# Kernel optimization log

Hardware: AMD Instinct MI355X
Metric: run time of the kernel (lower is better)

## Reference

```python
import jax, jax.numpy as jnp
import numpy as np


def setup_inputs() -> dict:
    key = jax.random.key(0)
    ks = jax.random.split(key, 7)
    E = 768; CH = 3; PS = 16; B = 128; P = 196
    return {
        "x": jax.random.normal(ks[0], (B, P, E), dtype=jnp.float32),
        "We": jax.random.normal(ks[1], (CH * PS * PS, E), dtype=jnp.float32) * (1.0 / np.sqrt(E)),
        "be": jax.random.normal(ks[2], (CH * PS * PS,), dtype=jnp.float32) * 0.01,
        "filter_re": jax.random.normal(ks[3], (1, 1, 1, PS, PS), dtype=jnp.float32),
        "filter_im": jax.random.normal(ks[4], (1, 1, 1, PS, PS), dtype=jnp.float32),
        "Wd": jax.random.normal(ks[5], (E, CH * PS * PS), dtype=jnp.float32) * (1.0 / np.sqrt(CH * PS * PS)),
        "bd": jax.random.normal(ks[6], (E,), dtype=jnp.float32) * 0.01,
        "ch": 3,
        "patch_size": 16,
    }


def reference(x, We, be, filter_re, filter_im, Wd, bd, ch, patch_size):
    # encode: [b,p,E] -> [b,p,ch*ps*ps]
    h = jnp.einsum('bpe,ce->bpc', x, We) + be
    b, p, _ = h.shape
    h = h.reshape(b, p, ch, patch_size, patch_size)
    # batched 2D FFT over the two trailing patch dims
    hf = jnp.fft.fft2(h, axes=(-2, -1))
    filt = (filter_re + 1j * filter_im).astype(hf.dtype)  # [1,1,1,ps,ps]
    r = jnp.fft.ifft2(hf * filt, axes=(-2, -1))
    a = jnp.abs(r).reshape(b, p, ch * patch_size * patch_size)
    # decode: [b,p,ch*ps*ps] -> [b,p,E]
    return jnp.einsum('bpc,ec->bpe', a, Wd) + bd
```

## Files before the change

kernel.cpp:

```cpp
#include <hip/hip_runtime.h>

typedef short short8 __attribute__((ext_vector_type(8)));
typedef unsigned short ushort8 __attribute__((ext_vector_type(8)));
typedef float f32x4 __attribute__((ext_vector_type(4)));

__device__ __forceinline__ unsigned short f32_to_bf16(float f) {
  unsigned u = __float_as_uint(f);
  unsigned r = 0x7fffu + ((u >> 16) & 1u);
  return (unsigned short)((u + r) >> 16);
}
__device__ __forceinline__ float bf16_to_f32(unsigned short h) {
  return __uint_as_float(((unsigned)h) << 16);
}

__global__ void cvt_f32_bf16(const float* __restrict__ s,
                             unsigned short* __restrict__ d, int n8) {
  int i = blockIdx.x * blockDim.x + threadIdx.x;
  if (i >= n8) return;
  const float4* sp = (const float4*)s;
  float4 a = sp[2 * i], b = sp[2 * i + 1];
  ushort8 o;
  o[0] = f32_to_bf16(a.x); o[1] = f32_to_bf16(a.y);
  o[2] = f32_to_bf16(a.z); o[3] = f32_to_bf16(a.w);
  o[4] = f32_to_bf16(b.x); o[5] = f32_to_bf16(b.y);
  o[6] = f32_to_bf16(b.z); o[7] = f32_to_bf16(b.w);
  ((ushort8*)d)[i] = o;
}

__device__ __forceinline__ void gload_lds16(const void* g, void* l) {
  auto* gp = (const __attribute__((address_space(1))) uint32_t*)((uintptr_t)g);
  auto* lp = (__attribute__((address_space(3))) uint32_t*)(uint32_t)(uintptr_t)l;
  __builtin_amdgcn_global_load_lds(gp, lp, 16, 0, 0);
}

template <int OUT_BF16>
__global__ __launch_bounds__(256) void gemm_bt(
    const unsigned short* __restrict__ A, const unsigned short* __restrict__ B,
    const float* __restrict__ bias, void* __restrict__ out,
    int M, int N, int K, int nbx) {
  __shared__ __align__(16) unsigned short As[2][128 * 64];
  __shared__ __align__(16) unsigned short Bs[2][128 * 64];

  const int tid = threadIdx.x;
  const int lane = tid & 63;
  const int wid = tid >> 6;
  const int wr = wid >> 1, wc = wid & 1;

  const int nwg = gridDim.x;
  const int cpx = nwg >> 3;
  const int bid = blockIdx.x;
  const int lid = (bid & 7) * cpx + (bid >> 3);
  const int m0 = (lid / nbx) * 128, n0 = (lid % nbx) * 128;

  const int lr8 = lane >> 3;
  const int swk = ((lane & 7) ^ lr8) * 8;

  f32x4 acc[4][4] = {};

  auto STAGE = [&](int buf, int k0) {
#pragma unroll
    for (int c = 0; c < 4; ++c) {
      const int rowc = wid * 32 + c * 8;
      gload_lds16(A + (size_t)(m0 + rowc + lr8) * K + (k0 + swk),
                  &As[buf][rowc * 64]);
      gload_lds16(B + (size_t)(n0 + rowc + lr8) * K + (k0 + swk),
                  &Bs[buf][rowc * 64]);
    }
  };

  const int rsel = lane & 15;
  auto COMPUTE = [&](int buf) {
#pragma unroll
    for (int ks = 0; ks < 2; ++ks) {
      const int kbyte = ks * 64 + (lane >> 4) * 16;
      short8 af[4], bf[4];
#pragma unroll
      for (int m = 0; m < 4; ++m) {
        const int row = wr * 64 + m * 16 + rsel;
        af[m] = *(const short8*)((const char*)&As[buf][0] +
                                 row * 128 + (kbyte ^ ((row & 7) << 4)));
      }
#pragma unroll
      for (int n = 0; n < 4; ++n) {
        const int row = wc * 64 + n * 16 + rsel;
        bf[n] = *(const short8*)((const char*)&Bs[buf][0] +
                                 row * 128 + (kbyte ^ ((row & 7) << 4)));
      }
#pragma unroll
      for (int m = 0; m < 4; ++m)
#pragma unroll
        for (int n = 0; n < 4; ++n)
          acc[m][n] = __builtin_amdgcn_mfma_f32_16x16x32_bf16(
              af[m], bf[n], acc[m][n], 0, 0, 0);
    }
  };

  const int nk = K >> 6;
  STAGE(0, 0);
  __syncthreads();
  int cur = 0;
  for (int t = 1; t < nk; ++t) {
    STAGE(cur ^ 1, t * 64);
    COMPUTE(cur);
    __syncthreads();
    cur ^= 1;
  }
  COMPUTE(cur);

  const int fr = lane & 15, fq = lane >> 4;
#pragma unroll
  for (int n = 0; n < 4; ++n) {
    const int gcol = n0 + wc * 64 + n * 16 + fr;
    const float bv = bias[gcol];
#pragma unroll
    for (int m = 0; m < 4; ++m) {
      const int grow = m0 + wr * 64 + m * 16 + fq * 4;
#pragma unroll
      for (int j = 0; j < 4; ++j) {
        float v = acc[m][n][j] + bv;
        if (OUT_BF16)
          ((unsigned short*)out)[(size_t)(grow + j) * N + gcol] = f32_to_bf16(v);
        else
          ((float*)out)[(size_t)(grow + j) * N + gcol] = v;
      }
    }
  }
}

constexpr float C16T[16] = {
    1.f,  0.9238795325112867f,  0.7071067811865476f,  0.3826834323650898f,
    0.f, -0.3826834323650898f, -0.7071067811865476f, -0.9238795325112867f,
   -1.f, -0.9238795325112867f, -0.7071067811865476f, -0.3826834323650898f,
    0.f,  0.3826834323650898f,  0.7071067811865476f,  0.9238795325112867f};
constexpr float S16T[16] = {
    0.f,  0.3826834323650898f,  0.7071067811865476f,  0.9238795325112867f,
    1.f,  0.9238795325112867f,  0.7071067811865476f,  0.3826834323650898f,
    0.f, -0.3826834323650898f, -0.7071067811865476f, -0.9238795325112867f,
   -1.f, -0.9238795325112867f, -0.7071067811865476f, -0.3826834323650898f};

__device__ __forceinline__ void dft16(const float* xr, const float* xi,
                                      float* Xr, float* Xi, const float sgn) {
  float Tr[4][4], Ti[4][4];
#pragma unroll
  for (int c0 = 0; c0 < 4; ++c0) {
    float ar = xr[c0],      ai = xi[c0];
    float br = xr[c0 + 4],  bi = xi[c0 + 4];
    float cr = xr[c0 + 8],  ci = xi[c0 + 8];
    float dr = xr[c0 + 12], di = xi[c0 + 12];
    float Er = ar + cr, Ei = ai + ci, Fr = ar - cr, Fi = ai - ci;
    float Gr = br + dr, Gi = bi + di, Hr = br - dr, Hi = bi - di;
    Tr[c0][0] = Er + Gr; Ti[c0][0] = Ei + Gi;
    Tr[c0][2] = Er - Gr; Ti[c0][2] = Ei - Gi;
    float wHr = -sgn * Hi, wHi = sgn * Hr;
    Tr[c0][1] = Fr + wHr; Ti[c0][1] = Fi + wHi;
    Tr[c0][3] = Fr - wHr; Ti[c0][3] = Fi - wHi;
  }
#pragma unroll
  for (int u = 0; u < 16; ++u) {
    const int m = u & 3;
    float sr = Tr[0][m], si = Ti[0][m];
#pragma unroll
    for (int c0 = 1; c0 < 4; ++c0) {
      const int k = (u * c0) & 15;
      const float wr = C16T[k];
      const float wi = sgn * S16T[k];
      sr += wr * Tr[c0][m] - wi * Ti[c0][m];
      si += wr * Ti[c0][m] + wi * Tr[c0][m];
    }
    Xr[u] = sr; Xi[u] = si;
  }
}

__global__ __launch_bounds__(256) void fft_filter(
    unsigned short* __restrict__ h, const float* __restrict__ fre,
    const float* __restrict__ fim) {
  __shared__ float2 S[16 * 276];
  const int tid = threadIdx.x;
  const int p = tid >> 4;
  const int q = tid & 15;
  const size_t gp = (size_t)blockIdx.x * 16 + p;
  const int sb = p * 276;

  {
    const unsigned short* row = h + gp * 256 + q * 16;
    ushort8 v0 = ((const ushort8*)row)[0];
    ushort8 v1 = ((const ushort8*)row)[1];
    float xr[16], xi[16], Xr[16], Xi[16];
#pragma unroll
    for (int j = 0; j < 8; ++j) {
      xr[j] = bf16_to_f32(v0[j]);
      xr[j + 8] = bf16_to_f32(v1[j]);
    }
#pragma unroll
    for (int j = 0; j < 16; ++j) xi[j] = 0.f;
    dft16(xr, xi, Xr, Xi, -1.f);
#pragma unroll
    for (int u = 0; u < 16; ++u) S[sb + q * 17 + u] = make_float2(Xr[u], Xi[u]);
  }
  __syncthreads();

  {
    float xr[16], xi[16], Xr[16], Xi[16];
#pragma unroll
    for (int k = 0; k < 16; ++k) {
      float2 t = S[sb + k * 17 + q];
      xr[k] = t.x; xi[k] = t.y;
    }
    dft16(xr, xi, Xr, Xi, -1.f);
#pragma unroll
    for (int v = 0; v < 16; ++v) {
      float fr = fre[v * 16 + q], fi = fim[v * 16 + q];
      float tr = Xr[v] * fr - Xi[v] * fi;
      float ti = Xr[v] * fi + Xi[v] * fr;
      xr[v] = tr; xi[v] = ti;
    }
    dft16(xr, xi, Xr, Xi, 1.f);
#pragma unroll
    for (int r = 0; r < 16; ++r) S[sb + r * 17 + q] = make_float2(Xr[r], Xi[r]);
  }
  __syncthreads();

  {
    float xr[16], xi[16], Xr[16], Xi[16];
#pragma unroll
    for (int u = 0; u < 16; ++u) {
      float2 t = S[sb + q * 17 + u];
      xr[u] = t.x; xi[u] = t.y;
    }
    dft16(xr, xi, Xr, Xi, 1.f);
    ushort8 o0, o1;
#pragma unroll
    for (int c = 0; c < 8; ++c) {
      float a0 = sqrtf(Xr[c] * Xr[c] + Xi[c] * Xi[c]) * (1.f / 256.f);
      float a1 = sqrtf(Xr[c + 8] * Xr[c + 8] + Xi[c + 8] * Xi[c + 8]) * (1.f / 256.f);
      o0[c] = f32_to_bf16(a0);
      o1[c] = f32_to_bf16(a1);
    }
    unsigned short* row = h + gp * 256 + q * 16;
    ((ushort8*)row)[0] = o0;
    ((ushort8*)row)[1] = o1;
  }
}

extern "C" void kernel_launch(void* const* d_in, const int* in_sizes, int n_in,
                              void* d_out, int out_size, void* d_ws,
                              size_t ws_size, hipStream_t stream) {
  const float* x   = (const float*)d_in[0];
  const float* We  = (const float*)d_in[1];
  const float* be  = (const float*)d_in[2];
  const float* fre = (const float*)d_in[3];
  const float* fim = (const float*)d_in[4];
  const float* Wd  = (const float*)d_in[5];
  const float* bd  = (const float*)d_in[6];

  const int E = 768, C = 768;
  const int nX = in_sizes[0];
  const int M  = nX / E;
  const int nW = E * C;

  char* w = (char*)d_ws;
  unsigned short* xb  = (unsigned short*)w;
  unsigned short* Web = (unsigned short*)(w + (size_t)nX * 2);
  unsigned short* Wdb = (unsigned short*)(w + (size_t)nX * 2 + (size_t)nW * 2);
  unsigned short* hb  = (unsigned short*)(w + (size_t)nX * 2 + (size_t)nW * 4);

  cvt_f32_bf16<<<(nX / 8 + 255) / 256, 256, 0, stream>>>(x, xb, nX / 8);
  cvt_f32_bf16<<<(nW / 8 + 255) / 256, 256, 0, stream>>>(We, Web, nW / 8);
  cvt_f32_bf16<<<(nW / 8 + 255) / 256, 256, 0, stream>>>(Wd, Wdb, nW / 8);

  const int nbx1 = C / 128;
  gemm_bt<1><<<nbx1 * (M / 128), 256, 0, stream>>>(xb, Web, be, hb, M, C, E, nbx1);

  fft_filter<<<(M * 3) / 16, 256, 0, stream>>>(hb, fre, fim);

  const int nbx2 = E / 128;
  gemm_bt<0><<<nbx2 * (M / 128), 256, 0, stream>>>(hb, Wdb, bd, (float*)d_out, M, E, C, nbx2);
}
```

Before: 156.1 us.

## Fold FFT filter into encoder weights and fuse magnitude into dual GEMM

The FFT-filter-IFFT chain is linear, so it is applied to the encoder weight columns and bias rather than to every activation patch. This produces complex (real and imaginary) weight matrices, and a dual-accumulator GEMM computes both parts and takes the magnitude in its epilogue. That removes the per-activation FFT kernel and its extra round trip through the h buffer. In exchange the encoder does twice the MFMA work, and the weight folding is recomputed on every call.

```diff
diff --git a/kernel.cpp b/kernel.cpp
--- a/kernel.cpp
+++ b/kernel.cpp
@@ -33,100 +33,6 @@
   __builtin_amdgcn_global_load_lds(gp, lp, 16, 0, 0);
 }
 
-template <int OUT_BF16>
-__global__ __launch_bounds__(256) void gemm_bt(
-    const unsigned short* __restrict__ A, const unsigned short* __restrict__ B,
-    const float* __restrict__ bias, void* __restrict__ out,
-    int M, int N, int K, int nbx) {
-  __shared__ __align__(16) unsigned short As[2][128 * 64];
-  __shared__ __align__(16) unsigned short Bs[2][128 * 64];
-
-  const int tid = threadIdx.x;
-  const int lane = tid & 63;
-  const int wid = tid >> 6;
-  const int wr = wid >> 1, wc = wid & 1;
-
-  const int nwg = gridDim.x;
-  const int cpx = nwg >> 3;
-  const int bid = blockIdx.x;
-  const int lid = (bid & 7) * cpx + (bid >> 3);
-  const int m0 = (lid / nbx) * 128, n0 = (lid % nbx) * 128;
-
-  const int lr8 = lane >> 3;
-  const int swk = ((lane & 7) ^ lr8) * 8;
-
-  f32x4 acc[4][4] = {};
-
-  auto STAGE = [&](int buf, int k0) {
-#pragma unroll
-    for (int c = 0; c < 4; ++c) {
-      const int rowc = wid * 32 + c * 8;
-      gload_lds16(A + (size_t)(m0 + rowc + lr8) * K + (k0 + swk),
-                  &As[buf][rowc * 64]);
-      gload_lds16(B + (size_t)(n0 + rowc + lr8) * K + (k0 + swk),
-                  &Bs[buf][rowc * 64]);
-    }
-  };
-
-  const int rsel = lane & 15;
-  auto COMPUTE = [&](int buf) {
-#pragma unroll
-    for (int ks = 0; ks < 2; ++ks) {
-      const int kbyte = ks * 64 + (lane >> 4) * 16;
-      short8 af[4], bf[4];
-#pragma unroll
-      for (int m = 0; m < 4; ++m) {
-        const int row = wr * 64 + m * 16 + rsel;
-        af[m] = *(const short8*)((const char*)&As[buf][0] +
-                                 row * 128 + (kbyte ^ ((row & 7) << 4)));
-      }
-#pragma unroll
-      for (int n = 0; n < 4; ++n) {
-        const int row = wc * 64 + n * 16 + rsel;
-        bf[n] = *(const short8*)((const char*)&Bs[buf][0] +
-                                 row * 128 + (kbyte ^ ((row & 7) << 4)));
-      }
-#pragma unroll
-      for (int m = 0; m < 4; ++m)
-#pragma unroll
-        for (int n = 0; n < 4; ++n)
-          acc[m][n] = __builtin_amdgcn_mfma_f32_16x16x32_bf16(
-              af[m], bf[n], acc[m][n], 0, 0, 0);
-    }
-  };
-
-  const int nk = K >> 6;
-  STAGE(0, 0);
-  __syncthreads();
-  int cur = 0;
-  for (int t = 1; t < nk; ++t) {
-    STAGE(cur ^ 1, t * 64);
-    COMPUTE(cur);
-    __syncthreads();
-    cur ^= 1;
-  }
-  COMPUTE(cur);
-
-  const int fr = lane & 15, fq = lane >> 4;
-#pragma unroll
-  for (int n = 0; n < 4; ++n) {
-    const int gcol = n0 + wc * 64 + n * 16 + fr;
-    const float bv = bias[gcol];
-#pragma unroll
-    for (int m = 0; m < 4; ++m) {
-      const int grow = m0 + wr * 64 + m * 16 + fq * 4;
-#pragma unroll
-      for (int j = 0; j < 4; ++j) {
-        float v = acc[m][n][j] + bv;
-        if (OUT_BF16)
-          ((unsigned short*)out)[(size_t)(grow + j) * N + gcol] = f32_to_bf16(v);
-        else
-          ((float*)out)[(size_t)(grow + j) * N + gcol] = v;
-      }
-    }
-  }
-}
-
 constexpr float C16T[16] = {
     1.f,  0.9238795325112867f,  0.7071067811865476f,  0.3826834323650898f,
     0.f, -0.3826834323650898f, -0.7071067811865476f, -0.9238795325112867f,
@@ -171,28 +77,30 @@
   }
 }
 
-__global__ __launch_bounds__(256) void fft_filter(
-    unsigned short* __restrict__ h, const float* __restrict__ fre,
-    const float* __restrict__ fim) {
+__global__ __launch_bounds__(256) void fold_filter(
+    const float* __restrict__ We, const float* __restrict__ be,
+    const float* __restrict__ fre, const float* __restrict__ fim,
+    unsigned short* __restrict__ Wre, unsigned short* __restrict__ Wim,
+    float* __restrict__ be_re, float* __restrict__ be_im) {
   __shared__ float2 S[16 * 276];
   const int tid = threadIdx.x;
   const int p = tid >> 4;
   const int q = tid & 15;
-  const size_t gp = (size_t)blockIdx.x * 16 + p;
+  const int item = blockIdx.x * 16 + p;
+  const bool isW = item < 2304;
+  const bool isB = (item >= 2304) && (item < 2307);
+  const int e = isW ? (item / 3) : 0;
+  const int ch = isW ? (item % 3) : (isB ? (item - 2304) : 0);
   const int sb = p * 276;
 
   {
-    const unsigned short* row = h + gp * 256 + q * 16;
-    ushort8 v0 = ((const ushort8*)row)[0];
-    ushort8 v1 = ((const ushort8*)row)[1];
     float xr[16], xi[16], Xr[16], Xi[16];
 #pragma unroll
-    for (int j = 0; j < 8; ++j) {
-      xr[j] = bf16_to_f32(v0[j]);
-      xr[j + 8] = bf16_to_f32(v1[j]);
-    }
-#pragma unroll
-    for (int j = 0; j < 16; ++j) xi[j] = 0.f;
+    for (int c = 0; c < 16; ++c) {
+      const int crow = ch * 256 + q * 16 + c;
+      xr[c] = isW ? We[(size_t)crow * 768 + e] : be[crow];
+      xi[c] = 0.f;
+    }
     dft16(xr, xi, Xr, Xi, -1.f);
 #pragma unroll
     for (int u = 0; u < 16; ++u) S[sb + q * 17 + u] = make_float2(Xr[u], Xi[u]);
@@ -228,17 +136,213 @@
       xr[u] = t.x; xi[u] = t.y;
     }
     dft16(xr, xi, Xr, Xi, 1.f);
-    ushort8 o0, o1;
-#pragma unroll
-    for (int c = 0; c < 8; ++c) {
-      float a0 = sqrtf(Xr[c] * Xr[c] + Xi[c] * Xi[c]) * (1.f / 256.f);
-      float a1 = sqrtf(Xr[c + 8] * Xr[c + 8] + Xi[c + 8] * Xi[c + 8]) * (1.f / 256.f);
-      o0[c] = f32_to_bf16(a0);
-      o1[c] = f32_to_bf16(a1);
-    }
-    unsigned short* row = h + gp * 256 + q * 16;
-    ((ushort8*)row)[0] = o0;
-    ((ushort8*)row)[1] = o1;
+#pragma unroll
+    for (int c = 0; c < 16; ++c) {
+      const int crow = ch * 256 + q * 16 + c;
+      const float rr = Xr[c] * (1.f / 256.f);
+      const float ri = Xi[c] * (1.f / 256.f);
+      if (isW) {
+        Wre[(size_t)crow * 768 + e] = f32_to_bf16(rr);
+        Wim[(size_t)crow * 768 + e] = f32_to_bf16(ri);
+      } else if (isB) {
+        be_re[crow] = rr;
+        be_im[crow] = ri;
+      }
+    }
+  }
+}
+
+__global__ __launch_bounds__(256) void gemm_enc_dual(
+    const unsigned short* __restrict__ A, const unsigned short* __restrict__ Bre,
+    const unsigned short* __restrict__ Bim, const float* __restrict__ be_re,
+    const float* __restrict__ be_im, unsigned short* __restrict__ out,
+    int M, int K, int nbx) {
+  __shared__ __align__(16) unsigned short As[2][128 * 64];
+  __shared__ __align__(16) unsigned short Rs[2][64 * 64];
+  __shared__ __align__(16) unsigned short Is[2][64 * 64];
+
+  const int tid = threadIdx.x;
+  const int lane = tid & 63;
+  const int wid = tid >> 6;
+  const int wr = wid >> 1, wc = wid & 1;
+
+  const int nwg = gridDim.x;
+  const int cpx = nwg >> 3;
+  const int bid = blockIdx.x;
+  const int lid = (bid & 7) * cpx + (bid >> 3);
+  const int m0 = (lid / nbx) * 128, n0 = (lid % nbx) * 64;
+
+  const int lr8 = lane >> 3;
+  const int swk = ((lane & 7) ^ lr8) * 8;
+
+  f32x4 accr[4][2] = {};
+  f32x4 acci[4][2] = {};
+
+  auto STAGE = [&](int buf, int k0) {
+#pragma unroll
+    for (int c = 0; c < 4; ++c) {
+      const int rowc = wid * 32 + c * 8;
+      gload_lds16(A + (size_t)(m0 + rowc + lr8) * K + (k0 + swk),
+                  &As[buf][rowc * 64]);
+    }
+#pragma unroll
+    for (int c = 0; c < 2; ++c) {
+      const int rowc = wid * 16 + c * 8;
+      gload_lds16(Bre + (size_t)(n0 + rowc + lr8) * K + (k0 + swk),
+                  &Rs[buf][rowc * 64]);
+      gload_lds16(Bim + (size_t)(n0 + rowc + lr8) * K + (k0 + swk),
+                  &Is[buf][rowc * 64]);
+    }
+  };
+
+  const int rsel = lane & 15;
+  auto COMPUTE = [&](int buf) {
+#pragma unroll
+    for (int ks = 0; ks < 2; ++ks) {
+      const int kbyte = ks * 64 + (lane >> 4) * 16;
+      short8 af[4], brf[2], bif[2];
+#pragma unroll
+      for (int m = 0; m < 4; ++m) {
+        const int row = wr * 64 + m * 16 + rsel;
+        af[m] = *(const short8*)((const char*)&As[buf][0] +
+                                 row * 128 + (kbyte ^ ((row & 7) << 4)));
+      }
+#pragma unroll
+      for (int n = 0; n < 2; ++n) {
+        const int row = wc * 32 + n * 16 + rsel;
+        brf[n] = *(const short8*)((const char*)&Rs[buf][0] +
+                                  row * 128 + (kbyte ^ ((row & 7) << 4)));
+        bif[n] = *(const short8*)((const char*)&Is[buf][0] +
+                                  row * 128 + (kbyte ^ ((row & 7) << 4)));
+      }
+#pragma unroll
+      for (int m = 0; m < 4; ++m)
+#pragma unroll
+        for (int n = 0; n < 2; ++n) {
+          accr[m][n] = __builtin_amdgcn_mfma_f32_16x16x32_bf16(
+              af[m], brf[n], accr[m][n], 0, 0, 0);
+          acci[m][n] = __builtin_amdgcn_mfma_f32_16x16x32_bf16(
+              af[m], bif[n], acci[m][n], 0, 0, 0);
+        }
+    }
+  };
+
+  const int nk = K >> 6;
+  STAGE(0, 0);
+  __syncthreads();
+  int cur = 0;
+  for (int t = 1; t < nk; ++t) {
+    STAGE(cur ^ 1, t * 64);
+    COMPUTE(cur);
+    __syncthreads();
+    cur ^= 1;
+  }
+  COMPUTE(cur);
+
+  const int fr = lane & 15, fq = lane >> 4;
+  const int N = 768;
+#pragma unroll
+  for (int n = 0; n < 2; ++n) {
+    const int gcol = n0 + wc * 32 + n * 16 + fr;
+    const float br = be_re[gcol], bi = be_im[gcol];
+#pragma unroll
+    for (int m = 0; m < 4; ++m) {
+      const int grow = m0 + wr * 64 + m * 16 + fq * 4;
+#pragma unroll
+      for (int j = 0; j < 4; ++j) {
+        const float re = accr[m][n][j] + br;
+        const float im = acci[m][n][j] + bi;
+        out[(size_t)(grow + j) * N + gcol] = f32_to_bf16(sqrtf(re * re + im * im));
+      }
+    }
+  }
+}
+
+__global__ __launch_bounds__(256) void gemm_bt(
+    const unsigned short* __restrict__ A, const unsigned short* __restrict__ B,
+    const float* __restrict__ bias, float* __restrict__ out,
+    int M, int N, int K, int nbx) {
+  __shared__ __align__(16) unsigned short As[2][128 * 64];
+  __shared__ __align__(16) unsigned short Bs[2][128 * 64];
+
+  const int tid = threadIdx.x;
+  const int lane = tid & 63;
+  const int wid = tid >> 6;
+  const int wr = wid >> 1, wc = wid & 1;
+
+  const int nwg = gridDim.x;
+  const int cpx = nwg >> 3;
+  const int bid = blockIdx.x;
+  const int lid = (bid & 7) * cpx + (bid >> 3);
+  const int m0 = (lid / nbx) * 128, n0 = (lid % nbx) * 128;
+
+  const int lr8 = lane >> 3;
+  const int swk = ((lane & 7) ^ lr8) * 8;
+
+  f32x4 acc[4][4] = {};
+
+  auto STAGE = [&](int buf, int k0) {
+#pragma unroll
+    for (int c = 0; c < 4; ++c) {
+      const int rowc = wid * 32 + c * 8;
+      gload_lds16(A + (size_t)(m0 + rowc + lr8) * K + (k0 + swk),
+                  &As[buf][rowc * 64]);
+      gload_lds16(B + (size_t)(n0 + rowc + lr8) * K + (k0 + swk),
+                  &Bs[buf][rowc * 64]);
+    }
+  };
+
+  const int rsel = lane & 15;
+  auto COMPUTE = [&](int buf) {
+#pragma unroll
+    for (int ks = 0; ks < 2; ++ks) {
+      const int kbyte = ks * 64 + (lane >> 4) * 16;
+      short8 af[4], bf[4];
+#pragma unroll
+      for (int m = 0; m < 4; ++m) {
+        const int row = wr * 64 + m * 16 + rsel;
+        af[m] = *(const short8*)((const char*)&As[buf][0] +
+                                 row * 128 + (kbyte ^ ((row & 7) << 4)));
+      }
+#pragma unroll
+      for (int n = 0; n < 4; ++n) {
+        const int row = wc * 64 + n * 16 + rsel;
+        bf[n] = *(const short8*)((const char*)&Bs[buf][0] +
+                                 row * 128 + (kbyte ^ ((row & 7) << 4)));
+      }
+#pragma unroll
+      for (int m = 0; m < 4; ++m)
+#pragma unroll
+        for (int n = 0; n < 4; ++n)
+          acc[m][n] = __builtin_amdgcn_mfma_f32_16x16x32_bf16(
+              af[m], bf[n], acc[m][n], 0, 0, 0);
+    }
+  };
+
+  const int nk = K >> 6;
+  STAGE(0, 0);
+  __syncthreads();
+  int cur = 0;
+  for (int t = 1; t < nk; ++t) {
+    STAGE(cur ^ 1, t * 64);
+    COMPUTE(cur);
+    __syncthreads();
+    cur ^= 1;
+  }
+  COMPUTE(cur);
+
+  const int fr = lane & 15, fq = lane >> 4;
+#pragma unroll
+  for (int n = 0; n < 4; ++n) {
+    const int gcol = n0 + wc * 64 + n * 16 + fr;
+    const float bv = bias[gcol];
+#pragma unroll
+    for (int m = 0; m < 4; ++m) {
+      const int grow = m0 + wr * 64 + m * 16 + fq * 4;
+#pragma unroll
+      for (int j = 0; j < 4; ++j)
+        out[(size_t)(grow + j) * N + gcol] = acc[m][n][j] + bv;
+    }
   }
 }
 
@@ -259,20 +363,24 @@
   const int nW = E * C;
 
   char* w = (char*)d_ws;
-  unsigned short* xb  = (unsigned short*)w;
-  unsigned short* Web = (unsigned short*)(w + (size_t)nX * 2);
-  unsigned short* Wdb = (unsigned short*)(w + (size_t)nX * 2 + (size_t)nW * 2);
-  unsigned short* hb  = (unsigned short*)(w + (size_t)nX * 2 + (size_t)nW * 4);
+  unsigned short* xb    = (unsigned short*)w;
+  unsigned short* Wdb   = (unsigned short*)(w + (size_t)nX * 2);
+  unsigned short* Wre   = Wdb + nW;
+  unsigned short* Wim   = Wre + nW;
+  float*          be_re = (float*)(Wim + nW);
+  float*          be_im = be_re + C;
+  unsigned short* hb    = (unsigned short*)(be_im + C);
 
   cvt_f32_bf16<<<(nX / 8 + 255) / 256, 256, 0, stream>>>(x, xb, nX / 8);
-  cvt_f32_bf16<<<(nW / 8 + 255) / 256, 256, 0, stream>>>(We, Web, nW / 8);
   cvt_f32_bf16<<<(nW / 8 + 255) / 256, 256, 0, stream>>>(Wd, Wdb, nW / 8);
 
-  const int nbx1 = C / 128;
-  gemm_bt<1><<<nbx1 * (M / 128), 256, 0, stream>>>(xb, Web, be, hb, M, C, E, nbx1);
-
-  fft_filter<<<(M * 3) / 16, 256, 0, stream>>>(hb, fre, fim);
+  fold_filter<<<145, 256, 0, stream>>>(We, be, fre, fim, Wre, Wim, be_re, be_im);
+
+  const int nbx1 = C / 64;
+  gemm_enc_dual<<<nbx1 * (M / 128), 256, 0, stream>>>(xb, Wre, Wim, be_re,
+                                                      be_im, hb, M, E, nbx1);
 
   const int nbx2 = E / 128;
-  gemm_bt<0><<<nbx2 * (M / 128), 256, 0, stream>>>(hb, Wdb, bd, (float*)d_out, M, E, C, nbx2);
-}
+  gemm_bt<<<nbx2 * (M / 128), 256, 0, stream>>>(hb, Wdb, bd, (float*)d_out, M,
+                                                E, C, nbx2);
+}
```

New measurement: 154.1 us. Within noise of the previous version (-1.3%).
